# Optimization experiments

Measured on AMD Instinct MI355X. Metric: run time of the kernel, lower is better.

Reference implementation:

```python
import jax, jax.numpy as jnp
import numpy as np

NUM_USERS = 100000
NUM_ITEMS = 100000
N = NUM_USERS + NUM_ITEMS
D = 64
E = 3200000


def setup_inputs() -> dict:
    key = jax.random.key(0)
    ks = jax.random.split(key, 8)
    edge_index = jax.random.randint(ks[0], (2, E), 0, N, dtype=jnp.int64)
    edge_weight = jax.random.uniform(ks[1], (E,), dtype=jnp.float32)
    user_emb = jax.random.normal(ks[2], (NUM_USERS, D), dtype=jnp.float32) * 0.1
    item_emb = jax.random.normal(ks[3], (NUM_ITEMS, D), dtype=jnp.float32) * 0.1
    s = 1.0 / np.sqrt(D)
    W1 = jax.random.uniform(ks[4], (D, D), dtype=jnp.float32, minval=-s, maxval=s)
    b1 = jax.random.uniform(ks[5], (D,), dtype=jnp.float32, minval=-s, maxval=s)
    W2 = jax.random.uniform(ks[6], (D, D), dtype=jnp.float32, minval=-s, maxval=s)
    b2 = jax.random.uniform(ks[7], (D,), dtype=jnp.float32, minval=-s, maxval=s)
    return {"edge_index": edge_index, "edge_weight": edge_weight,
            "user_emb": user_emb, "item_emb": item_emb,
            "W1": W1, "b1": b1, "W2": W2, "b2": b2}


def _gcn_layer(x, src, dst, edge_weight, W, b):
    # message: edge_weight * x[src]; aggregate: scatter-add at dst
    msg = edge_weight[:, None] * x[src]              # [E, D] gather + mul
    agg = jax.ops.segment_sum(msg, dst, num_segments=N)  # [N, D] scatter-add
    updated = (agg + x) * 0.5                        # residual average
    return updated @ W + b                           # linear


def reference(edge_index, edge_weight, user_emb, item_emb, W1, b1, W2, b2):
    src = edge_index[0]
    dst = edge_index[1]
    x = jnp.concatenate([user_emb, item_emb], axis=0)  # [N, D]
    x = _gcn_layer(x, src, dst, edge_weight, W1, b1)
    x = _gcn_layer(x, src, dst, edge_weight, W2, b2)
    return x
```

## Files before the change

### kernel.cpp

```cpp
#include <hip/hip_runtime.h>
#include <hip/hip_fp16.h>

#define NUM_USERS 100000
#define NN        200000
#define DD        64
#define EE        3200000
#define SCAN_CHUNK 2048
#define NB_SCAN   98

#define KB_   391
#define GSEG  512
#define EPS   (EE / GSEG)
#define MSEG  (KB_ * GSEG)

typedef _Float16 half8 __attribute__((ext_vector_type(8)));
typedef _Float16 half4 __attribute__((ext_vector_type(4)));
typedef float    f32x4 __attribute__((ext_vector_type(4)));

__global__ __launch_bounds__(256) void scan_partials_kernel(
    const int* __restrict__ counts, int* __restrict__ bsum, int len)
{
    __shared__ int s[256];
    const int t = threadIdx.x;
    int sum = 0;
    for (int i = t; i < SCAN_CHUNK; i += 256) {
        const int idx = blockIdx.x * SCAN_CHUNK + i;
        sum += (idx < len) ? counts[idx] : 0;
    }
    s[t] = sum; __syncthreads();
    for (int off = 128; off > 0; off >>= 1) {
        if (t < off) s[t] += s[t + off];
        __syncthreads();
    }
    if (t == 0) bsum[blockIdx.x] = s[0];
}

__global__ __launch_bounds__(128) void scan_top_kernel(int* __restrict__ bsum, int nb)
{
    __shared__ int s[128];
    const int t = threadIdx.x;
    const int v = (t < nb) ? bsum[t] : 0;
    s[t] = v; __syncthreads();
    for (int off = 1; off < 128; off <<= 1) {
        int add = (t >= off) ? s[t - off] : 0;
        __syncthreads();
        s[t] += add;
        __syncthreads();
    }
    if (t < nb) bsum[t] = s[t] - v;
}

__global__ __launch_bounds__(256) void scan_write_kernel(
    const int* __restrict__ counts, const int* __restrict__ bsum,
    int* __restrict__ out, int len)
{
    __shared__ int s[256];
    const int t    = threadIdx.x;
    const int base = blockIdx.x * SCAN_CHUNK + t * 8;
    int c[8], ex[8], run = 0;
#pragma unroll
    for (int j = 0; j < 8; ++j) {
        const int idx = base + j;
        c[j] = (idx < len) ? counts[idx] : 0;
        ex[j] = run; run += c[j];
    }
    s[t] = run; __syncthreads();
    for (int off = 1; off < 256; off <<= 1) {
        int add = (t >= off) ? s[t - off] : 0;
        __syncthreads();
        s[t] += add;
        __syncthreads();
    }
    const int thread_base = bsum[blockIdx.x] + s[t] - run;
#pragma unroll
    for (int j = 0; j < 8; ++j) {
        const int idx = base + j;
        if (idx < len) out[idx] = thread_base + ex[j];
    }
}

__global__ __launch_bounds__(256) void seg_hist_kernel(
    const int* __restrict__ ei, int* __restrict__ counts_seg)
{
    __shared__ int h[KB_];
    const int s = blockIdx.x;
    for (int k = threadIdx.x; k < KB_; k += 256) h[k] = 0;
    __syncthreads();
    const int base = s * EPS;
    for (int i = threadIdx.x; i < EPS; i += 256) {
        const int dst = __builtin_nontemporal_load(&ei[EE + base + i]);
        atomicAdd(&h[dst >> 9], 1);
    }
    __syncthreads();
    for (int k = threadIdx.x; k < KB_; k += 256)
        counts_seg[k * GSEG + s] = h[k];
}

__global__ __launch_bounds__(256) void append_kernel(
    const int* __restrict__ ei, const float* __restrict__ ew,
    const int* __restrict__ bofs, int2* __restrict__ etmp)
{
    __shared__ int fr[KB_];
    const int s = blockIdx.x;
    for (int k = threadIdx.x; k < KB_; k += 256) fr[k] = bofs[k * GSEG + s];
    __syncthreads();
    const int base = s * EPS;
    for (int i = threadIdx.x; i < EPS; i += 256) {
        const int e   = base + i;
        const int   src = __builtin_nontemporal_load(&ei[e]);
        const int   dst = __builtin_nontemporal_load(&ei[EE + e]);
        const float w   = __builtin_nontemporal_load(&ew[e]);
        const int k  = dst >> 9;
        const int dl = dst & 511;
        const int pos = atomicAdd(&fr[k], 1);
        etmp[pos] = make_int2(src | (dl << 18), __float_as_int(w));
    }
}

__global__ __launch_bounds__(256) void bucket_sort_kernel(
    const int2* __restrict__ etmp, const int* __restrict__ bofs,
    int2* __restrict__ edges, int* __restrict__ row_ptr)
{
    __shared__ int cnt[512];
    __shared__ int cur[512];
    __shared__ int part[256];
    const int k = blockIdx.x;
    const int t = threadIdx.x;
    cnt[t] = 0; cnt[t + 256] = 0;
    __syncthreads();
    const int beg = bofs[k * GSEG];
    const int end = (k == KB_ - 1) ? EE : bofs[(k + 1) * GSEG];
    for (int e = beg + t; e < end; e += 256)
        atomicAdd(&cnt[((unsigned)etmp[e].x) >> 18], 1);
    __syncthreads();
    const int c0 = cnt[2 * t], c1 = cnt[2 * t + 1];
    const int run = c0 + c1;
    part[t] = run; __syncthreads();
    for (int off = 1; off < 256; off <<= 1) {
        int add = (t >= off) ? part[t - off] : 0;
        __syncthreads();
        part[t] += add;
        __syncthreads();
    }
    const int base = beg + part[t] - run;
    cur[2 * t]     = base;
    cur[2 * t + 1] = base + c0;
    const int node0 = (k << 9) + 2 * t;
    if (node0 < NN)     row_ptr[node0]     = base;
    if (node0 + 1 < NN) row_ptr[node0 + 1] = base + c0;
    if (k == KB_ - 1 && t == 0) row_ptr[NN] = EE;
    __syncthreads();
    for (int e = beg + t; e < end; e += 256) {
        const int2 r  = etmp[e];
        const int  dl = ((unsigned)r.x) >> 18;
        const int  pos = atomicAdd(&cur[dl], 1);
        edges[pos] = make_int2((r.x & 0x3FFFF) << 7, r.y);
    }
}

__global__ __launch_bounds__(256) void convert_x_kernel(
    const float* __restrict__ xu, const float* __restrict__ xi,
    _Float16* __restrict__ xh)
{
    const int i = blockIdx.x * 256 + threadIdx.x;
    if (i >= NN * DD / 4) return;
    const float4 v = (i < NUM_USERS * DD / 4)
                       ? ((const float4*)xu)[i]
                       : ((const float4*)xi)[i - NUM_USERS * DD / 4];
    half4 o; o[0] = (_Float16)v.x; o[1] = (_Float16)v.y;
             o[2] = (_Float16)v.z; o[3] = (_Float16)v.w;
    ((half4*)xh)[i] = o;
}

__global__ __launch_bounds__(256) void convert_w_kernel(
    const float* __restrict__ W1, const float* __restrict__ W2,
    _Float16* __restrict__ Wt)
{
    const int idx = blockIdx.x * 256 + threadIdx.x;
    if (idx >= 2 * DD * DD) return;
    const int mat = idx >> 12, rem = idx & 4095, k = rem >> 6, n = rem & 63;
    const float* W = mat ? W2 : W1;
    Wt[mat * DD * DD + n * DD + k] = (_Float16)W[k * DD + n];
}

__global__ __launch_bounds__(256) void aggregate_kernel(
    const int2* __restrict__ edges, const int* __restrict__ row_ptr,
    const _Float16* __restrict__ xh, _Float16* __restrict__ u)
{
    const int wave = (blockIdx.x * 256 + threadIdx.x) >> 6;
    const int lane = threadIdx.x & 63;
    const unsigned lane2 = lane * 2;
    const int n0 = wave * 2;
    const int n1 = n0 + 1;
    const char* xb = (const char*)xh;

    float acc0 = (float)*(const _Float16*)(xb + ((unsigned)n0 << 7) + lane2);
    float acc1 = (float)*(const _Float16*)(xb + ((unsigned)n1 << 7) + lane2);

    int       e0   = row_ptr[n0];
    const int end0 = row_ptr[n1];
    int       e1   = end0;
    const int end1 = row_ptr[n1 + 1];

    while (e0 + 4 <= end0 && e1 + 4 <= end1) {
        const int2 a0 = edges[e0 + 0], a1 = edges[e0 + 1];
        const int2 a2 = edges[e0 + 2], a3 = edges[e0 + 3];
        const int2 b0 = edges[e1 + 0], b1 = edges[e1 + 1];
        const int2 b2 = edges[e1 + 2], b3 = edges[e1 + 3];
        const float va0 = (float)*(const _Float16*)(xb + (unsigned)a0.x + lane2);
        const float va1 = (float)*(const _Float16*)(xb + (unsigned)a1.x + lane2);
        const float va2 = (float)*(const _Float16*)(xb + (unsigned)a2.x + lane2);
        const float va3 = (float)*(const _Float16*)(xb + (unsigned)a3.x + lane2);
        const float vb0 = (float)*(const _Float16*)(xb + (unsigned)b0.x + lane2);
        const float vb1 = (float)*(const _Float16*)(xb + (unsigned)b1.x + lane2);
        const float vb2 = (float)*(const _Float16*)(xb + (unsigned)b2.x + lane2);
        const float vb3 = (float)*(const _Float16*)(xb + (unsigned)b3.x + lane2);
        acc0 = fmaf(__int_as_float(a0.y), va0, acc0);
        acc0 = fmaf(__int_as_float(a1.y), va1, acc0);
        acc0 = fmaf(__int_as_float(a2.y), va2, acc0);
        acc0 = fmaf(__int_as_float(a3.y), va3, acc0);
        acc1 = fmaf(__int_as_float(b0.y), vb0, acc1);
        acc1 = fmaf(__int_as_float(b1.y), vb1, acc1);
        acc1 = fmaf(__int_as_float(b2.y), vb2, acc1);
        acc1 = fmaf(__int_as_float(b3.y), vb3, acc1);
        e0 += 4; e1 += 4;
    }
    for (; e0 + 4 <= end0; e0 += 4) {
        const int2 a0 = edges[e0 + 0], a1 = edges[e0 + 1];
        const int2 a2 = edges[e0 + 2], a3 = edges[e0 + 3];
        const float va0 = (float)*(const _Float16*)(xb + (unsigned)a0.x + lane2);
        const float va1 = (float)*(const _Float16*)(xb + (unsigned)a1.x + lane2);
        const float va2 = (float)*(const _Float16*)(xb + (unsigned)a2.x + lane2);
        const float va3 = (float)*(const _Float16*)(xb + (unsigned)a3.x + lane2);
        acc0 = fmaf(__int_as_float(a0.y), va0, acc0);
        acc0 = fmaf(__int_as_float(a1.y), va1, acc0);
        acc0 = fmaf(__int_as_float(a2.y), va2, acc0);
        acc0 = fmaf(__int_as_float(a3.y), va3, acc0);
    }
    for (; e0 < end0; ++e0) {
        const int2 p = edges[e0];
        acc0 = fmaf(__int_as_float(p.y),
                    (float)*(const _Float16*)(xb + (unsigned)p.x + lane2), acc0);
    }
    for (; e1 + 4 <= end1; e1 += 4) {
        const int2 b0 = edges[e1 + 0], b1 = edges[e1 + 1];
        const int2 b2 = edges[e1 + 2], b3 = edges[e1 + 3];
        const float vb0 = (float)*(const _Float16*)(xb + (unsigned)b0.x + lane2);
        const float vb1 = (float)*(const _Float16*)(xb + (unsigned)b1.x + lane2);
        const float vb2 = (float)*(const _Float16*)(xb + (unsigned)b2.x + lane2);
        const float vb3 = (float)*(const _Float16*)(xb + (unsigned)b3.x + lane2);
        acc1 = fmaf(__int_as_float(b0.y), vb0, acc1);
        acc1 = fmaf(__int_as_float(b1.y), vb1, acc1);
        acc1 = fmaf(__int_as_float(b2.y), vb2, acc1);
        acc1 = fmaf(__int_as_float(b3.y), vb3, acc1);
    }
    for (; e1 < end1; ++e1) {
        const int2 p = edges[e1];
        acc1 = fmaf(__int_as_float(p.y),
                    (float)*(const _Float16*)(xb + (unsigned)p.x + lane2), acc1);
    }

    char* ub = (char*)u;
    *(_Float16*)(ub + ((unsigned)n0 << 7) + lane2) = (_Float16)(acc0 * 0.5f);
    *(_Float16*)(ub + ((unsigned)n1 << 7) + lane2) = (_Float16)(acc1 * 0.5f);
}

template<bool HALF_OUT>
__global__ __launch_bounds__(256) void gemm64_kernel(
    const _Float16* __restrict__ u, const _Float16* __restrict__ Wt,
    const float* __restrict__ bias, void* __restrict__ outp)
{
    const int wid  = blockIdx.x * 4 + (threadIdx.x >> 6);
    const int lane = threadIdx.x & 63;
    const int m    = lane & 15;
    const int quad = lane >> 4;
    const size_t rowbase = (size_t)wid * 16;

    half8 bf[4][2];
#pragma unroll
    for (int c = 0; c < 4; ++c)
#pragma unroll
        for (int h = 0; h < 2; ++h)
            bf[c][h] = *(const half8*)(Wt + (size_t)(c * 16 + m) * DD + h * 32 + quad * 8);

    const half8 a0 = *(const half8*)(u + (rowbase + m) * DD +  0 + quad * 8);
    const half8 a1 = *(const half8*)(u + (rowbase + m) * DD + 32 + quad * 8);

    f32x4 acc[4];
#pragma unroll
    for (int c = 0; c < 4; ++c) {
        f32x4 z = {0.f, 0.f, 0.f, 0.f};
        z = __builtin_amdgcn_mfma_f32_16x16x32_f16(a0, bf[c][0], z, 0, 0, 0);
        z = __builtin_amdgcn_mfma_f32_16x16x32_f16(a1, bf[c][1], z, 0, 0, 0);
        acc[c] = z;
    }

#pragma unroll
    for (int c = 0; c < 4; ++c) {
        const float bv = bias[c * 16 + m];
#pragma unroll
        for (int r = 0; r < 4; ++r) {
            const size_t row = rowbase + quad * 4 + r;
            const float val = acc[c][r] + bv;
            if (HALF_OUT) ((_Float16*)outp)[row * DD + c * 16 + m] = (_Float16)val;
            else          ((float*)    outp)[row * DD + c * 16 + m] = val;
        }
    }
}

extern "C" void kernel_launch(void* const* d_in, const int* in_sizes, int n_in,
                              void* d_out, int out_size, void* d_ws, size_t ws_size,
                              hipStream_t stream) {
    const int*   edge_index  = (const int*)  d_in[0];
    const float* edge_weight = (const float*)d_in[1];
    const float* user_emb    = (const float*)d_in[2];
    const float* item_emb    = (const float*)d_in[3];
    const float* W1          = (const float*)d_in[4];
    const float* b1          = (const float*)d_in[5];
    const float* W2          = (const float*)d_in[6];
    const float* b2          = (const float*)d_in[7];
    float*       out         = (float*)d_out;

    char* ws = (char*)d_ws;
    _Float16* xh        = (_Float16*)(ws);
    _Float16* u         = (_Float16*)(ws + 25600000);
    int2*     etmp      = (int2*)    (ws + 25600000);
    int2*     edges     = (int2*)    (ws + 51200000);
    int*      row_ptr   = (int*)     (ws + 76800000);
    int*      cseg      = (int*)     (ws + 78400064);
    int*      bofs      = (int*)     (ws + 79200832);
    int*      bsum      = (int*)     (ws + 80001600);
    _Float16* Wt        = (_Float16*)(ws + 80002112);

    const int gemm_blocks = (NN / 16) / 4;
    const int agg_blocks  = NN / 8;

    seg_hist_kernel     <<<GSEG,    256, 0, stream>>>(edge_index, cseg);
    scan_partials_kernel<<<NB_SCAN, 256, 0, stream>>>(cseg, bsum, MSEG);
    scan_top_kernel     <<<1,       128, 0, stream>>>(bsum, NB_SCAN);
    scan_write_kernel   <<<NB_SCAN, 256, 0, stream>>>(cseg, bsum, bofs, MSEG);

    append_kernel      <<<GSEG, 256, 0, stream>>>(edge_index, edge_weight, bofs, etmp);
    bucket_sort_kernel <<<KB_,  256, 0, stream>>>(etmp, bofs, edges, row_ptr);

    convert_x_kernel<<<(NN * DD / 4 + 255) / 256, 256, 0, stream>>>(user_emb, item_emb, xh);
    convert_w_kernel<<<(2 * DD * DD + 255) / 256, 256, 0, stream>>>(W1, W2, Wt);

    aggregate_kernel<<<agg_blocks, 256, 0, stream>>>(edges, row_ptr, xh, u);
    gemm64_kernel<true><<<gemm_blocks, 256, 0, stream>>>(u, Wt, b1, (void*)xh);

    aggregate_kernel<<<agg_blocks, 256, 0, stream>>>(edges, row_ptr, xh, u);
    gemm64_kernel<false><<<gemm_blocks, 256, 0, stream>>>(u, Wt + DD * DD, b2, (void*)out);
}
```

Before: 491.0 us.

## Process four nodes per wave with a merged, double-buffered edge stream in aggregation

Each wave in the aggregation kernel now handles four consecutive CSR rows and treats their edges as one contiguous range. It walks that range in groups of eight, with two register buffers so the edge and feature loads for the next group are issued before the current group is accumulated. A group that crosses a row boundary is routed to the right accumulator with per-edge selects. The intent is to keep more gathers in flight and avoid the many tail loops of the per-row scheme, at the cost of more registers and select arithmetic at row boundaries.

```diff
diff --git a/kernel.cpp b/kernel.cpp
--- a/kernel.cpp
+++ b/kernel.cpp
@@ -183,6 +183,52 @@
     Wt[mat * DD * DD + n * DD + k] = (_Float16)W[k * DD + n];
 }
 
+
+#define LOADG(r, h, basev)                                                   \
+  do {                                                                       \
+    _Pragma("unroll")                                                        \
+    for (int j = 0; j < 8; ++j) {                                            \
+      int idx = (basev) + j;                                                 \
+      idx = idx < end ? idx : end - 1;                                       \
+      idx = idx > 0 ? idx : 0;                                               \
+      r[j] = edges[idx];                                                     \
+      h[j] = *(const _Float16*)(xb + (unsigned)r[j].x + lane2);              \
+    }                                                                        \
+  } while (0)
+
+#define FMA8(r, h, a)                                                        \
+  do {                                                                       \
+    _Pragma("unroll")                                                        \
+    for (int j = 0; j < 8; ++j)                                              \
+      a = fmaf(__int_as_float(r[j].y), (float)h[j], a);                      \
+  } while (0)
+
+#define PROCESS(r, h, basev)                                                 \
+  do {                                                                       \
+    const int selL = ((basev) >= f0) + ((basev) >= f1) + ((basev) >= f2);    \
+    const int selH = ((basev) + 7 >= f0) + ((basev) + 7 >= f1) +             \
+                     ((basev) + 7 >= f2);                                    \
+    if (selL == selH && (basev) + 8 <= end) {                                \
+      if      (selL == 0) { FMA8(r, h, acc0); }                              \
+      else if (selL == 1) { FMA8(r, h, acc1); }                              \
+      else if (selL == 2) { FMA8(r, h, acc2); }                              \
+      else                { FMA8(r, h, acc3); }                              \
+    } else {                                                                 \
+      _Pragma("unroll")                                                      \
+      for (int j = 0; j < 8; ++j) {                                          \
+        const int idx = (basev) + j;                                         \
+        float w = __int_as_float(r[j].y);                                    \
+        w = (idx < end) ? w : 0.0f;                                          \
+        const int sel = (idx >= f0) + (idx >= f1) + (idx >= f2);             \
+        const float hv = (float)h[j];                                        \
+        acc0 = fmaf((sel == 0) ? w : 0.0f, hv, acc0);                        \
+        acc1 = fmaf((sel == 1) ? w : 0.0f, hv, acc1);                        \
+        acc2 = fmaf((sel == 2) ? w : 0.0f, hv, acc2);                        \
+        acc3 = fmaf((sel == 3) ? w : 0.0f, hv, acc3);                        \
+      }                                                                      \
+    }                                                                        \
+  } while (0)
+
 __global__ __launch_bounds__(256) void aggregate_kernel(
     const int2* __restrict__ edges, const int* __restrict__ row_ptr,
     const _Float16* __restrict__ xh, _Float16* __restrict__ u)
@@ -190,79 +236,41 @@
     const int wave = (blockIdx.x * 256 + threadIdx.x) >> 6;
     const int lane = threadIdx.x & 63;
     const unsigned lane2 = lane * 2;
-    const int n0 = wave * 2;
-    const int n1 = n0 + 1;
+    const int nbase = wave * 4;
     const char* xb = (const char*)xh;
 
-    float acc0 = (float)*(const _Float16*)(xb + ((unsigned)n0 << 7) + lane2);
-    float acc1 = (float)*(const _Float16*)(xb + ((unsigned)n1 << 7) + lane2);
-
-    int       e0   = row_ptr[n0];
-    const int end0 = row_ptr[n1];
-    int       e1   = end0;
-    const int end1 = row_ptr[n1 + 1];
-
-    while (e0 + 4 <= end0 && e1 + 4 <= end1) {
-        const int2 a0 = edges[e0 + 0], a1 = edges[e0 + 1];
-        const int2 a2 = edges[e0 + 2], a3 = edges[e0 + 3];
-        const int2 b0 = edges[e1 + 0], b1 = edges[e1 + 1];
-        const int2 b2 = edges[e1 + 2], b3 = edges[e1 + 3];
-        const float va0 = (float)*(const _Float16*)(xb + (unsigned)a0.x + lane2);
-        const float va1 = (float)*(const _Float16*)(xb + (unsigned)a1.x + lane2);
-        const float va2 = (float)*(const _Float16*)(xb + (unsigned)a2.x + lane2);
-        const float va3 = (float)*(const _Float16*)(xb + (unsigned)a3.x + lane2);
-        const float vb0 = (float)*(const _Float16*)(xb + (unsigned)b0.x + lane2);
-        const float vb1 = (float)*(const _Float16*)(xb + (unsigned)b1.x + lane2);
-        const float vb2 = (float)*(const _Float16*)(xb + (unsigned)b2.x + lane2);
-        const float vb3 = (float)*(const _Float16*)(xb + (unsigned)b3.x + lane2);
-        acc0 = fmaf(__int_as_float(a0.y), va0, acc0);
-        acc0 = fmaf(__int_as_float(a1.y), va1, acc0);
-        acc0 = fmaf(__int_as_float(a2.y), va2, acc0);
-        acc0 = fmaf(__int_as_float(a3.y), va3, acc0);
-        acc1 = fmaf(__int_as_float(b0.y), vb0, acc1);
-        acc1 = fmaf(__int_as_float(b1.y), vb1, acc1);
-        acc1 = fmaf(__int_as_float(b2.y), vb2, acc1);
-        acc1 = fmaf(__int_as_float(b3.y), vb3, acc1);
-        e0 += 4; e1 += 4;
-    }
-    for (; e0 + 4 <= end0; e0 += 4) {
-        const int2 a0 = edges[e0 + 0], a1 = edges[e0 + 1];
-        const int2 a2 = edges[e0 + 2], a3 = edges[e0 + 3];
-        const float va0 = (float)*(const _Float16*)(xb + (unsigned)a0.x + lane2);
-        const float va1 = (float)*(const _Float16*)(xb + (unsigned)a1.x + lane2);
-        const float va2 = (float)*(const _Float16*)(xb + (unsigned)a2.x + lane2);
-        const float va3 = (float)*(const _Float16*)(xb + (unsigned)a3.x + lane2);
-        acc0 = fmaf(__int_as_float(a0.y), va0, acc0);
-        acc0 = fmaf(__int_as_float(a1.y), va1, acc0);
-        acc0 = fmaf(__int_as_float(a2.y), va2, acc0);
-        acc0 = fmaf(__int_as_float(a3.y), va3, acc0);
-    }
-    for (; e0 < end0; ++e0) {
-        const int2 p = edges[e0];
-        acc0 = fmaf(__int_as_float(p.y),
-                    (float)*(const _Float16*)(xb + (unsigned)p.x + lane2), acc0);
-    }
-    for (; e1 + 4 <= end1; e1 += 4) {
-        const int2 b0 = edges[e1 + 0], b1 = edges[e1 + 1];
-        const int2 b2 = edges[e1 + 2], b3 = edges[e1 + 3];
-        const float vb0 = (float)*(const _Float16*)(xb + (unsigned)b0.x + lane2);
-        const float vb1 = (float)*(const _Float16*)(xb + (unsigned)b1.x + lane2);
-        const float vb2 = (float)*(const _Float16*)(xb + (unsigned)b2.x + lane2);
-        const float vb3 = (float)*(const _Float16*)(xb + (unsigned)b3.x + lane2);
-        acc1 = fmaf(__int_as_float(b0.y), vb0, acc1);
-        acc1 = fmaf(__int_as_float(b1.y), vb1, acc1);
-        acc1 = fmaf(__int_as_float(b2.y), vb2, acc1);
-        acc1 = fmaf(__int_as_float(b3.y), vb3, acc1);
-    }
-    for (; e1 < end1; ++e1) {
-        const int2 p = edges[e1];
-        acc1 = fmaf(__int_as_float(p.y),
-                    (float)*(const _Float16*)(xb + (unsigned)p.x + lane2), acc1);
+    const int beg = __builtin_amdgcn_readfirstlane(row_ptr[nbase + 0]);
+    const int f0  = __builtin_amdgcn_readfirstlane(row_ptr[nbase + 1]);
+    const int f1  = __builtin_amdgcn_readfirstlane(row_ptr[nbase + 2]);
+    const int f2  = __builtin_amdgcn_readfirstlane(row_ptr[nbase + 3]);
+    const int end = __builtin_amdgcn_readfirstlane(row_ptr[nbase + 4]);
+
+    float acc0 = (float)*(const _Float16*)(xb + ((unsigned)(nbase + 0) << 7) + lane2);
+    float acc1 = (float)*(const _Float16*)(xb + ((unsigned)(nbase + 1) << 7) + lane2);
+    float acc2 = (float)*(const _Float16*)(xb + ((unsigned)(nbase + 2) << 7) + lane2);
+    float acc3 = (float)*(const _Float16*)(xb + ((unsigned)(nbase + 3) << 7) + lane2);
+
+    int2     rA[8], rB[8];
+    _Float16 hA[8], hB[8];
+
+    int g = beg;
+    LOADG(rA, hA, g);
+    LOADG(rB, hB, g + 8);
+    while (g < end) {
+        PROCESS(rA, hA, g);
+        if (g + 16 < end) LOADG(rA, hA, g + 16);
+        g += 8;
+        if (g >= end) break;
+        PROCESS(rB, hB, g);
+        if (g + 16 < end) LOADG(rB, hB, g + 16);
+        g += 8;
     }
 
     char* ub = (char*)u;
-    *(_Float16*)(ub + ((unsigned)n0 << 7) + lane2) = (_Float16)(acc0 * 0.5f);
-    *(_Float16*)(ub + ((unsigned)n1 << 7) + lane2) = (_Float16)(acc1 * 0.5f);
+    *(_Float16*)(ub + ((unsigned)(nbase + 0) << 7) + lane2) = (_Float16)(acc0 * 0.5f);
+    *(_Float16*)(ub + ((unsigned)(nbase + 1) << 7) + lane2) = (_Float16)(acc1 * 0.5f);
+    *(_Float16*)(ub + ((unsigned)(nbase + 2) << 7) + lane2) = (_Float16)(acc2 * 0.5f);
+    *(_Float16*)(ub + ((unsigned)(nbase + 3) << 7) + lane2) = (_Float16)(acc3 * 0.5f);
 }
 
 template<bool HALF_OUT>
@@ -333,7 +341,7 @@
     _Float16* Wt        = (_Float16*)(ws + 80002112);
 
     const int gemm_blocks = (NN / 16) / 4;
-    const int agg_blocks  = NN / 8;
+    const int agg_blocks  = NN / 16;
 
     seg_hist_kernel     <<<GSEG,    256, 0, stream>>>(edge_index, cseg);
     scan_partials_kernel<<<NB_SCAN, 256, 0, stream>>>(cseg, bsum, MSEG);
```

New measurement: 547.5 us. 1.12x slower.
